# Performance work log

Hardware: AMD Instinct MI355X
Metric: run time of the kernel (lower is better)

The kernel has to match this reference:

```python
import jax, jax.numpy as jnp
import numpy as np

V, E, L, D, B, S = 50000, 512, 1024, 10, 1024, 50
N_NODES = L - 1  # internal Huffman nodes (balanced tree from uniform label counts)
LN_EPS = 1e-5
N_HIDDEN = 10


def _build_tree():
    # balanced binary tree in heap order: node at depth t for leaf l is (2^t - 1) + (l >> (D - t))
    l = np.arange(L)[:, None]
    t = np.arange(D)[None, :]
    bits = ((l >> (D - 1 - t)) & 1).astype(np.int32)          # [L, D] path direction bits
    paths = ((2 ** t - 1) + (l >> (D - t))).astype(np.int32)  # [L, D] internal node ids
    return paths, bits


def setup_inputs() -> dict:
    key = jax.random.key(0)
    k1, k2, k3, k4, k5, k6 = jax.random.split(key, 6)
    paths, bits = _build_tree()
    return {
        "input_ids": jax.random.randint(k1, (B, S), 0, V),
        "emb_table": jax.random.normal(k2, (V, E), dtype=jnp.float32) * 0.02,
        "W_h": jax.random.normal(k3, (E, E), dtype=jnp.float32) * (1.0 / np.sqrt(E)),
        "b_h": jax.random.normal(k4, (E,), dtype=jnp.float32) * 0.01,
        "theta_W": jax.random.normal(k5, (N_NODES, E, 2), dtype=jnp.float32) * (1.0 / np.sqrt(E)),
        "theta_b": jax.random.normal(k6, (N_NODES, 2), dtype=jnp.float32) * 0.01,
        "paths": jnp.asarray(paths),
        "bits": jnp.asarray(bits),
    }


def reference(input_ids, emb_table, W_h, b_h, theta_W, theta_b, paths, bits):
    # embedding + mean pool over sequence
    x = jnp.take(emb_table, input_ids, axis=0).mean(axis=1)  # [B, E]
    # LayerNorm with default (non-learned) affine, created fresh in torch forward
    mu = x.mean(axis=-1, keepdims=True)
    var = x.var(axis=-1, keepdims=True)
    x = (x - mu) * jax.lax.rsqrt(var + LN_EPS)
    # repeated hidden linear (same weights, hidden_num times)
    for _ in range(N_HIDDEN):
        x = x @ W_h + b_h
    # hierarchical softmax: batched 2-way logits at every internal node
    logits = jnp.einsum('be,ned->bnd', x, theta_W) + theta_b  # [B, N, 2]
    probs = jax.nn.softmax(logits, axis=-1)                   # [B, N, 2]
    # gather each class's path probs and multiply along the path
    p = probs[:, paths, bits]                                  # [B, L, D]
    return jnp.prod(p, axis=-1)                                # [B, L]
```

## Files before the change

kernel.cpp:

```cpp
#include <hip/hip_runtime.h>
#include <hip/hip_bf16.h>
#include <math.h>

#define B_  1024
#define S_  50
#define E_  512
#define L_  1024
#define D_  10
#define NN  1023
#define LN_EPS 1e-5f
#define CBLK 72

typedef short short8 __attribute__((ext_vector_type(8)));
typedef float f32x4  __attribute__((ext_vector_type(4)));
typedef unsigned short u16;
typedef unsigned int   u32;

union PackU { unsigned int u[4]; short8 s; };

__device__ inline void split8(const float r[8], short8& hi, short8& lo) {
    PackU H, L;
#pragma unroll
    for (int q = 0; q < 4; ++q) {
        const unsigned int u0 = __float_as_uint(r[2*q+0]);
        const unsigned int u1 = __float_as_uint(r[2*q+1]);
        H.u[q] = (u0 >> 16) | (u1 & 0xFFFF0000u);
        const float h0 = __uint_as_float(u0 & 0xFFFF0000u);
        const float h1 = __uint_as_float(u1 & 0xFFFF0000u);
        const float l0 = r[2*q+0] - h0;
        const float l1 = r[2*q+1] - h1;
        unsigned int p;
        asm("v_cvt_pk_bf16_f32 %0, %1, %2" : "=v"(p) : "v"(l0), "v"(l1));
        L.u[q] = p;
    }
    hi = H.s; lo = L.s;
}

__device__ inline void split1(float v, u16& h, u16& l) {
    const unsigned int u = __float_as_uint(v);
    h = (u16)(u >> 16);
    const float hf = __uint_as_float(u & 0xFFFF0000u);
    const float lo = v - hf;
    unsigned int p;
    asm("v_cvt_pk_bf16_f32 %0, %1, %2" : "=v"(p) : "v"(lo), "v"(lo));
    l = (u16)(p & 0xFFFFu);
}

__device__ inline void split2(float v0, float v1, u32& hw, u32& lw) {
    const unsigned int u0 = __float_as_uint(v0);
    const unsigned int u1 = __float_as_uint(v1);
    hw = (u0 >> 16) | (u1 & 0xFFFF0000u);
    const float h0 = __uint_as_float(u0 & 0xFFFF0000u);
    const float h1 = __uint_as_float(u1 & 0xFFFF0000u);
    const float l0 = v0 - h0;
    const float l1 = v1 - h1;
    asm("v_cvt_pk_bf16_f32 %0, %1, %2" : "=v"(lw) : "v"(l0), "v"(l1));
}

struct BFrag { short8 ah[2], al[2], bh[2], bl[2]; };

__device__ inline void loadB(BFrag& f,
                             const u16* pah0, const u16* pal0,
                             const u16* pah1, const u16* pal1,
                             const u16* pbh0, const u16* pbl0,
                             const u16* pbh1, const u16* pbl1, int off) {
    f.ah[0] = *reinterpret_cast<const short8*>(pah0 + off);
    f.al[0] = *reinterpret_cast<const short8*>(pal0 + off);
    f.ah[1] = *reinterpret_cast<const short8*>(pah1 + off);
    f.al[1] = *reinterpret_cast<const short8*>(pal1 + off);
    f.bh[0] = *reinterpret_cast<const short8*>(pbh0 + off);
    f.bl[0] = *reinterpret_cast<const short8*>(pbl0 + off);
    f.bh[1] = *reinterpret_cast<const short8*>(pbh1 + off);
    f.bl[1] = *reinterpret_cast<const short8*>(pbl1 + off);
}

template<int TERMS>
__device__ inline void compB(const BFrag& f, f32x4 acc[2][2]) {
#pragma unroll
    for (int i = 0; i < 2; ++i)
#pragma unroll
        for (int j = 0; j < 2; ++j) {
            acc[i][j] = __builtin_amdgcn_mfma_f32_16x16x32_bf16(f.ah[i], f.bh[j], acc[i][j], 0, 0, 0);
            acc[i][j] = __builtin_amdgcn_mfma_f32_16x16x32_bf16(f.ah[i], f.bl[j], acc[i][j], 0, 0, 0);
            acc[i][j] = __builtin_amdgcn_mfma_f32_16x16x32_bf16(f.al[i], f.bh[j], acc[i][j], 0, 0, 0);
            if (TERMS == 4)
                acc[i][j] = __builtin_amdgcn_mfma_f32_16x16x32_bf16(f.al[i], f.bl[j], acc[i][j], 0, 0, 0);
        }
}

template<int TERMS>
__device__ inline void gemmB(const u16* pah0, const u16* pal0,
                             const u16* pah1, const u16* pal1,
                             const u16* pbh0, const u16* pbl0,
                             const u16* pbh1, const u16* pbl1,
                             f32x4 acc[2][2]) {
    BFrag f0, f1;
    loadB(f0, pah0, pal0, pah1, pal1, pbh0, pbl0, pbh1, pbl1, 0);
#pragma unroll 1
    for (int kt = 0; kt < 16; kt += 2) {
        loadB(f1, pah0, pal0, pah1, pal1, pbh0, pbl0, pbh1, pbl1, (kt + 1) * 32);
        compB<TERMS>(f0, acc);
        if (kt + 2 < 16) loadB(f0, pah0, pal0, pah1, pal1, pbh0, pbl0, pbh1, pbl1, (kt + 2) * 32);
        compB<TERMS>(f1, acc);
    }
}

__device__ inline void do_embed_row(const int* __restrict__ ids,
                                    const float* __restrict__ emb,
                                    u16* __restrict__ xah, u16* __restrict__ xal, int b) {
    const int t = threadIdx.x;
    float a0 = 0.f, a1 = 0.f;
    const int* idr = ids + b * S_;
#pragma unroll 5
    for (int s = 0; s < S_; ++s) {
        const float2 v = *reinterpret_cast<const float2*>(emb + (long)idr[s] * E_ + 2 * t);
        a0 += v.x;
        a1 += v.y;
    }
    a0 *= (1.f / S_);
    a1 *= (1.f / S_);

    __shared__ float red[256];
    red[t] = a0 + a1;
    __syncthreads();
    for (int off = 128; off > 0; off >>= 1) {
        if (t < off) red[t] += red[t + off];
        __syncthreads();
    }
    const float mean = red[0] * (1.f / E_);
    __syncthreads();
    const float d0 = a0 - mean, d1 = a1 - mean;
    red[t] = d0 * d0 + d1 * d1;
    __syncthreads();
    for (int off = 128; off > 0; off >>= 1) {
        if (t < off) red[t] += red[t + off];
        __syncthreads();
    }
    const float var = red[0] * (1.f / E_);
    const float inv = 1.f / sqrtf(var + LN_EPS);
    u32 hw, lw;
    split2(d0 * inv, d1 * inv, hw, lw);
    *reinterpret_cast<u32*>(xah + (long)b * E_ + 2 * t) = hw;
    *reinterpret_cast<u32*>(xal + (long)b * E_ + 2 * t) = lw;
}

__device__ inline void do_dpack(const float* __restrict__ thW,
                                u16* __restrict__ Dh, u16* __restrict__ Dl, int part) {
    const int total = NN * 256;
    const int nth = 64 * 256;
    for (int p = part * 256 + (int)threadIdx.x; p < total; p += nth) {
        const int n = p >> 8;
        const int kp = p & 255;
        const float4 v = *reinterpret_cast<const float4*>(thW + (long)n * 1024 + kp * 4);
        u32 hw, lw;
        split2(v.y - v.x, v.w - v.z, hw, lw);
        *reinterpret_cast<u32*>(Dh + (long)n * E_ + kp * 2) = hw;
        *reinterpret_cast<u32*>(Dl + (long)n * E_ + kp * 2) = lw;
    }
}

__device__ inline void compose_epilogue(f32x4 acc[2][2], int row_base, int col_base,
                                        int kg, int r_lo,
                                        const float* __restrict__ Bbias,
                                        u16* __restrict__ Ch, u16* __restrict__ Cl,
                                        u16* __restrict__ Th, u16* __restrict__ Tl,
                                        float* __restrict__ cvec) {
#pragma unroll
    for (int j = 0; j < 2; ++j) {
        const int col = col_base + j * 16 + r_lo;
        const float bb = Bbias[col];
#pragma unroll
        for (int i = 0; i < 2; ++i) {
            const int row0 = row_base + i * 16 + kg * 4;
            union { ushort4 v; u16 e[4]; } th, tl;
#pragma unroll
            for (int r2 = 0; r2 < 4; ++r2) {
                const int row = row0 + r2;
                float v = acc[i][j][r2];
                if (row == E_) { v += bb; cvec[col] = v; }
                u16 h, l;
                split1(v, h, l);
                if (row <= E_ && Ch != nullptr) {
                    Ch[(long)row * E_ + col] = h;
                    Cl[(long)row * E_ + col] = l;
                }
                th.e[r2] = h; tl.e[r2] = l;
            }
            if (row0 + 3 < E_) {
                *reinterpret_cast<ushort4*>(Th + (long)col * E_ + row0) = th.v;
                *reinterpret_cast<ushort4*>(Tl + (long)col * E_ + row0) = tl.v;
            }
        }
    }
}

__device__ inline void do_compose0(const float* __restrict__ Wh, const float* __restrict__ bh,
                                   u16* __restrict__ Ch, u16* __restrict__ Cl,
                                   u16* __restrict__ Th, u16* __restrict__ Tl,
                                   float* __restrict__ cvec, int bid) {
    const int tid  = threadIdx.x;
    const int wid  = tid >> 6;
    const int lane = tid & 63;
    const int r_lo = lane & 15;
    const int kg   = lane >> 4;
    const int row_base = (bid >> 3) * 64 + (wid >> 1) * 32;
    const int col_base = (bid & 7) * 64 + (wid & 1) * 32;
    f32x4 acc[2][2] = {};
#pragma unroll 2
    for (int kt = 0; kt < E_; kt += 32) {
        const int ks = kt + kg * 8;
        short8 ah[2], al[2], bhf[2], blf[2];
#pragma unroll
        for (int i = 0; i < 2; ++i) {
            const int row = row_base + i * 16 + r_lo;
            const float* ap = (row < E_) ? (Wh + (long)row * E_ + ks) : (bh + ks);
            const float4 v0 = *reinterpret_cast<const float4*>(ap);
            const float4 v1 = *reinterpret_cast<const float4*>(ap + 4);
            const float rr[8] = {v0.x, v0.y, v0.z, v0.w, v1.x, v1.y, v1.z, v1.w};
            split8(rr, ah[i], al[i]);
        }
#pragma unroll
        for (int j = 0; j < 2; ++j) {
            const int c = col_base + j * 16 + r_lo;
            float rr[8];
#pragma unroll
            for (int q = 0; q < 8; ++q) rr[q] = Wh[(long)(ks + q) * E_ + c];
            split8(rr, bhf[j], blf[j]);
        }
#pragma unroll
        for (int i = 0; i < 2; ++i)
#pragma unroll
            for (int j = 0; j < 2; ++j) {
                acc[i][j] = __builtin_amdgcn_mfma_f32_16x16x32_bf16(ah[i], bhf[j], acc[i][j], 0, 0, 0);
                acc[i][j] = __builtin_amdgcn_mfma_f32_16x16x32_bf16(ah[i], blf[j], acc[i][j], 0, 0, 0);
                acc[i][j] = __builtin_amdgcn_mfma_f32_16x16x32_bf16(al[i], bhf[j], acc[i][j], 0, 0, 0);
                acc[i][j] = __builtin_amdgcn_mfma_f32_16x16x32_bf16(al[i], blf[j], acc[i][j], 0, 0, 0);
            }
    }
    compose_epilogue(acc, row_base, col_base, kg, r_lo, bh, Ch, Cl, Th, Tl, cvec);
}

__device__ inline void do_composeB(const u16* __restrict__ Ah, const u16* __restrict__ Al,
                                   const u16* __restrict__ Bh, const u16* __restrict__ Bl,
                                   const float* __restrict__ Bbias,
                                   u16* __restrict__ Ch, u16* __restrict__ Cl,
                                   u16* __restrict__ Th, u16* __restrict__ Tl,
                                   float* __restrict__ cvec, int bid) {
    const int tid  = threadIdx.x;
    const int wid  = tid >> 6;
    const int lane = tid & 63;
    const int r_lo = lane & 15;
    const int kg   = lane >> 4;
    const int row_base = (bid >> 3) * 64 + (wid >> 1) * 32;
    const int col_base = (bid & 7) * 64 + (wid & 1) * 32;

    int ra0 = row_base + r_lo;        if (ra0 > E_) ra0 = E_;
    int ra1 = row_base + 16 + r_lo;   if (ra1 > E_) ra1 = E_;
    const long rb0 = col_base + r_lo;
    const long rb1 = col_base + 16 + r_lo;

    f32x4 acc[2][2] = {};
    gemmB<4>(Ah + (long)ra0 * E_ + kg * 8, Al + (long)ra0 * E_ + kg * 8,
             Ah + (long)ra1 * E_ + kg * 8, Al + (long)ra1 * E_ + kg * 8,
             Bh + rb0 * E_ + kg * 8,       Bl + rb0 * E_ + kg * 8,
             Bh + rb1 * E_ + kg * 8,       Bl + rb1 * E_ + kg * 8, acc);

    compose_epilogue(acc, row_base, col_base, kg, r_lo, Bbias, Ch, Cl, Th, Tl, cvec);
}

__device__ inline void do_applyB(const u16* __restrict__ Xh, const u16* __restrict__ Xl,
                                 const u16* __restrict__ Mh, const u16* __restrict__ Ml,
                                 const float* __restrict__ cvec,
                                 u16* __restrict__ Yh, u16* __restrict__ Yl,
                                 int tr, int tc) {
    const int tid  = threadIdx.x;
    const int wid  = tid >> 6;
    const int lane = tid & 63;
    const int r_lo = lane & 15;
    const int kg   = lane >> 4;
    const int row_base = tr * 64 + (wid >> 1) * 32;
    const int col_base = tc * 64 + (wid & 1) * 32;

    const long ra0 = row_base + r_lo;
    const long ra1 = row_base + 16 + r_lo;
    const long rb0 = col_base + r_lo;
    const long rb1 = col_base + 16 + r_lo;

    f32x4 acc[2][2] = {};
    gemmB<3>(Xh + ra0 * E_ + kg * 8, Xl + ra0 * E_ + kg * 8,
             Xh + ra1 * E_ + kg * 8, Xl + ra1 * E_ + kg * 8,
             Mh + rb0 * E_ + kg * 8, Ml + rb0 * E_ + kg * 8,
             Mh + rb1 * E_ + kg * 8, Ml + rb1 * E_ + kg * 8, acc);

#pragma unroll
    for (int j = 0; j < 2; ++j) {
        const int col = col_base + j * 16 + r_lo;
        const float bb = cvec[col];
#pragma unroll
        for (int i = 0; i < 2; ++i) {
#pragma unroll
            for (int r2 = 0; r2 < 4; ++r2) {
                const int row = row_base + i * 16 + kg * 4 + r2;
                u16 h, l;
                split1(acc[i][j][r2] + bb, h, l);
                Yh[(long)row * E_ + col] = h;
                Yl[(long)row * E_ + col] = l;
            }
        }
    }
}

__global__ __launch_bounds__(256) void k_fused0(const float* __restrict__ Wh,
                                                const float* __restrict__ bh,
                                                u16* __restrict__ Ch0, u16* __restrict__ Cl0,
                                                u16* __restrict__ Th0, u16* __restrict__ Tl0,
                                                float* __restrict__ cvec0,
                                                const int* __restrict__ ids,
                                                const float* __restrict__ emb,
                                                u16* __restrict__ xah, u16* __restrict__ xal,
                                                const float* __restrict__ thW,
                                                u16* __restrict__ Dh, u16* __restrict__ Dl) {
    const int bid = blockIdx.x;
    if (bid < CBLK)             do_compose0(Wh, bh, Ch0, Cl0, Th0, Tl0, cvec0, bid);
    else if (bid < CBLK + 1024) do_embed_row(ids, emb, xah, xal, bid - CBLK);
    else                        do_dpack(thW, Dh, Dl, bid - CBLK - 1024);
}

__global__ __launch_bounds__(256) void k_fused1(const u16* __restrict__ Ch0, const u16* __restrict__ Cl0,
                                                const u16* __restrict__ Th0, const u16* __restrict__ Tl0,
                                                const float* __restrict__ cvec0,
                                                u16* __restrict__ Th1, u16* __restrict__ Tl1,
                                                float* __restrict__ cvec1,
                                                const u16* __restrict__ xah, const u16* __restrict__ xal,
                                                u16* __restrict__ y1h, u16* __restrict__ y1l) {
    const int bid = blockIdx.x;
    if (bid < CBLK) {
        do_composeB(Ch0, Cl0, Th0, Tl0, cvec0, nullptr, nullptr, Th1, Tl1, cvec1, bid);
    } else {
        const int t = bid - CBLK;
        do_applyB(xah, xal, Th0, Tl0, cvec0, y1h, y1l, t >> 3, t & 7);
    }
}

__global__ __launch_bounds__(256) void k_apply(const u16* __restrict__ Yh, const u16* __restrict__ Yl,
                                               const u16* __restrict__ Th1, const u16* __restrict__ Tl1,
                                               const float* __restrict__ cvec1,
                                               u16* __restrict__ Zh, u16* __restrict__ Zl) {
    do_applyB(Yh, Yl, Th1, Tl1, cvec1, Zh, Zl, blockIdx.x >> 3, blockIdx.x & 7);
}

__global__ __launch_bounds__(256) void k_theta_sig(const u16* __restrict__ Xh, const u16* __restrict__ Xl,
                                                   const u16* __restrict__ Dh, const u16* __restrict__ Dl,
                                                   const float* __restrict__ thb,
                                                   float* __restrict__ sig) {
    const int tid  = threadIdx.x;
    const int wid  = tid >> 6;
    const int lane = tid & 63;
    const int r_lo = lane & 15;
    const int kg   = lane >> 4;
    const int tr = blockIdx.x >> 4;
    const int tc = blockIdx.x & 15;
    const int row_base = tr * 64 + (wid >> 1) * 32;
    const int col_base = tc * 64 + (wid & 1) * 32;

    long c0 = col_base + r_lo;        if (c0 > NN - 1) c0 = NN - 1;
    long c1 = col_base + 16 + r_lo;   if (c1 > NN - 1) c1 = NN - 1;
    const long ra0 = row_base + r_lo;
    const long ra1 = row_base + 16 + r_lo;

    f32x4 acc[2][2] = {};
    gemmB<3>(Xh + ra0 * E_ + kg * 8, Xl + ra0 * E_ + kg * 8,
             Xh + ra1 * E_ + kg * 8, Xl + ra1 * E_ + kg * 8,
             Dh + c0 * E_ + kg * 8,  Dl + c0 * E_ + kg * 8,
             Dh + c1 * E_ + kg * 8,  Dl + c1 * E_ + kg * 8, acc);

#pragma unroll
    for (int j = 0; j < 2; ++j) {
        const int col = col_base + j * 16 + r_lo;
        const int cc = (col > NN - 1) ? (NN - 1) : col;
        const float g = thb[2 * cc + 1] - thb[2 * cc + 0];
#pragma unroll
        for (int i = 0; i < 2; ++i) {
#pragma unroll
            for (int r2 = 0; r2 < 4; ++r2) {
                const int row = row_base + i * 16 + kg * 4 + r2;
                if (col < NN) {
                    const float z = acc[i][j][r2] + g;
                    sig[(long)row * 1024 + col] = 1.f / (1.f + __expf(-z));
                }
            }
        }
    }
}

__global__ __launch_bounds__(256) void k_leaf_gather(const float* __restrict__ sig,
                                                     float* __restrict__ out) {
    __shared__ float s[1024];
    const int b = blockIdx.x;
    const int tid = threadIdx.x;
    reinterpret_cast<float4*>(s)[tid] =
        reinterpret_cast<const float4*>(sig + (long)b * 1024)[tid];
    __syncthreads();
    float* orow = out + (long)b * L_;
#pragma unroll 1
    for (int q = 0; q < 4; ++q) {
        const int l = q * 256 + tid;
        float p = 1.f;
#pragma unroll
        for (int t = 0; t < D_; ++t) {
            const int node = (1 << t) - 1 + (l >> (D_ - t));
            const int bit  = (l >> (D_ - 1 - t)) & 1;
            const float sv = s[node];
            p *= bit ? sv : (1.f - sv);
        }
        orow[l] = p;
    }
}

extern "C" void kernel_launch(void* const* d_in, const int* in_sizes, int n_in,
                              void* d_out, int out_size, void* d_ws, size_t ws_size,
                              hipStream_t stream) {
    const int*   ids = (const int*)d_in[0];
    const float* emb = (const float*)d_in[1];
    const float* Wh  = (const float*)d_in[2];
    const float* bh  = (const float*)d_in[3];
    const float* thW = (const float*)d_in[4];
    const float* thb = (const float*)d_in[5];
    float* out = (float*)d_out;

    char* ws = (char*)d_ws;
    const size_t MB = 1u << 20;
    u16* xah = (u16*)(ws + 0 * MB);
    u16* xal = (u16*)(ws + 1 * MB);
    u16* y1h = (u16*)(ws + 2 * MB);
    u16* y1l = (u16*)(ws + 3 * MB);
    u16* y2h = (u16*)(ws + 4 * MB);
    u16* y2l = (u16*)(ws + 5 * MB);
    u16* y3h = (u16*)(ws + 6 * MB);
    u16* y3l = (u16*)(ws + 7 * MB);
    float* sig = (float*)(ws + 8 * MB);
    u16* Dh  = (u16*)(ws + 12 * MB);
    u16* Dl  = (u16*)(ws + 13 * MB);
    u16* Ch0 = (u16*)(ws + 14 * MB);
    u16* Cl0 = (u16*)(ws + 15 * MB);
    u16* Th0 = (u16*)(ws + 16 * MB);
    u16* Tl0 = (u16*)(ws + 16 * MB + 512 * 1024);
    u16* Th1 = (u16*)(ws + 17 * MB);
    u16* Tl1 = (u16*)(ws + 17 * MB + 512 * 1024);
    float* cvec0 = (float*)(ws + 18 * MB);
    float* cvec1 = (float*)(ws + 18 * MB + 4096);

    k_fused0<<<CBLK + 1024 + 64, 256, 0, stream>>>(Wh, bh, Ch0, Cl0, Th0, Tl0, cvec0,
                                                   ids, emb, xah, xal, thW, Dh, Dl);

    k_fused1<<<CBLK + 128, 256, 0, stream>>>(Ch0, Cl0, Th0, Tl0, cvec0,
                                             Th1, Tl1, cvec1,
                                             xah, xal, y1h, y1l);

    k_apply<<<128, 256, 0, stream>>>(y1h, y1l, Th1, Tl1, cvec1, y2h, y2l);

    k_apply<<<128, 256, 0, stream>>>(y2h, y2l, Th1, Tl1, cvec1, y3h, y3l);

    k_theta_sig<<<256, 256, 0, stream>>>(y3h, y3l, Dh, Dl, thb, sig);

    k_leaf_gather<<<B_, 256, 0, stream>>>(sig, out);
}
```

Baseline: 100.5 us.

## Split-K the apply and theta GEMMs into two halves with fp32 partial outputs

The apply and theta GEMMs now split K=512 into two halves, doubling the block count (128→256, 256→512) so more CUs are busy. Each half writes an fp32 partial, and the next stage sums the two partials and splits to bf16 hi/lo inside the GEMM load path. The theta bias is precomputed into gvec and the sigmoid moves into the leaf-gather kernel, which sums the partials. This trades higher occupancy for twice the fp32 intermediate traffic and extra conversion work in each GEMM.

Result: slower. 108.5 us (+7.9%).

```diff
diff --git a/kernel.cpp b/kernel.cpp
--- a/kernel.cpp
+++ b/kernel.cpp
@@ -88,7 +88,7 @@
         }
 }
 
-template<int TERMS>
+template<int TERMS, int CHUNKS>
 __device__ inline void gemmB(const u16* pah0, const u16* pal0,
                              const u16* pah1, const u16* pal1,
                              const u16* pbh0, const u16* pbl0,
@@ -97,11 +97,68 @@
     BFrag f0, f1;
     loadB(f0, pah0, pal0, pah1, pal1, pbh0, pbl0, pbh1, pbl1, 0);
 #pragma unroll 1
-    for (int kt = 0; kt < 16; kt += 2) {
+    for (int kt = 0; kt < CHUNKS; kt += 2) {
         loadB(f1, pah0, pal0, pah1, pal1, pbh0, pbl0, pbh1, pbl1, (kt + 1) * 32);
         compB<TERMS>(f0, acc);
-        if (kt + 2 < 16) loadB(f0, pah0, pal0, pah1, pal1, pbh0, pbl0, pbh1, pbl1, (kt + 2) * 32);
+        if (kt + 2 < CHUNKS) loadB(f0, pah0, pal0, pah1, pal1, pbh0, pbl0, pbh1, pbl1, (kt + 2) * 32);
         compB<TERMS>(f1, acc);
+    }
+}
+
+struct FPFrag { float aA[2][8], aB[2][8]; short8 bh[2], bl[2]; };
+
+__device__ inline void loadFP(FPFrag& f,
+                              const float* pa0A, const float* pa0B,
+                              const float* pa1A, const float* pa1B,
+                              const u16* pbh0, const u16* pbl0,
+                              const u16* pbh1, const u16* pbl1, int off) {
+    *reinterpret_cast<float4*>(&f.aA[0][0]) = *reinterpret_cast<const float4*>(pa0A + off);
+    *reinterpret_cast<float4*>(&f.aA[0][4]) = *reinterpret_cast<const float4*>(pa0A + off + 4);
+    *reinterpret_cast<float4*>(&f.aB[0][0]) = *reinterpret_cast<const float4*>(pa0B + off);
+    *reinterpret_cast<float4*>(&f.aB[0][4]) = *reinterpret_cast<const float4*>(pa0B + off + 4);
+    *reinterpret_cast<float4*>(&f.aA[1][0]) = *reinterpret_cast<const float4*>(pa1A + off);
+    *reinterpret_cast<float4*>(&f.aA[1][4]) = *reinterpret_cast<const float4*>(pa1A + off + 4);
+    *reinterpret_cast<float4*>(&f.aB[1][0]) = *reinterpret_cast<const float4*>(pa1B + off);
+    *reinterpret_cast<float4*>(&f.aB[1][4]) = *reinterpret_cast<const float4*>(pa1B + off + 4);
+    f.bh[0] = *reinterpret_cast<const short8*>(pbh0 + off);
+    f.bl[0] = *reinterpret_cast<const short8*>(pbl0 + off);
+    f.bh[1] = *reinterpret_cast<const short8*>(pbh1 + off);
+    f.bl[1] = *reinterpret_cast<const short8*>(pbl1 + off);
+}
+
+__device__ inline void compFP(const FPFrag& f, f32x4 acc[2][2]) {
+    short8 ah[2], al[2];
+#pragma unroll
+    for (int i = 0; i < 2; ++i) {
+        float rr[8];
+#pragma unroll
+        for (int q = 0; q < 8; ++q) rr[q] = f.aA[i][q] + f.aB[i][q];
+        split8(rr, ah[i], al[i]);
+    }
+#pragma unroll
+    for (int i = 0; i < 2; ++i)
+#pragma unroll
+        for (int j = 0; j < 2; ++j) {
+            acc[i][j] = __builtin_amdgcn_mfma_f32_16x16x32_bf16(ah[i], f.bh[j], acc[i][j], 0, 0, 0);
+            acc[i][j] = __builtin_amdgcn_mfma_f32_16x16x32_bf16(ah[i], f.bl[j], acc[i][j], 0, 0, 0);
+            acc[i][j] = __builtin_amdgcn_mfma_f32_16x16x32_bf16(al[i], f.bh[j], acc[i][j], 0, 0, 0);
+        }
+}
+
+template<int CHUNKS>
+__device__ inline void gemmFP(const float* pa0A, const float* pa0B,
+                              const float* pa1A, const float* pa1B,
+                              const u16* pbh0, const u16* pbl0,
+                              const u16* pbh1, const u16* pbl1,
+                              f32x4 acc[2][2]) {
+    FPFrag f0, f1;
+    loadFP(f0, pa0A, pa0B, pa1A, pa1B, pbh0, pbl0, pbh1, pbl1, 0);
+#pragma unroll 1
+    for (int kt = 0; kt < CHUNKS; kt += 2) {
+        loadFP(f1, pa0A, pa0B, pa1A, pa1B, pbh0, pbl0, pbh1, pbl1, (kt + 1) * 32);
+        compFP(f0, acc);
+        if (kt + 2 < CHUNKS) loadFP(f0, pa0A, pa0B, pa1A, pa1B, pbh0, pbl0, pbh1, pbl1, (kt + 2) * 32);
+        compFP(f1, acc);
     }
 }
 
@@ -145,10 +202,16 @@
 }
 
 __device__ inline void do_dpack(const float* __restrict__ thW,
-                                u16* __restrict__ Dh, u16* __restrict__ Dl, int part) {
+                                u16* __restrict__ Dh, u16* __restrict__ Dl,
+                                const float* __restrict__ thb,
+                                float* __restrict__ gvec, int part) {
+    const int tid = threadIdx.x;
+    const int p0 = part * 256 + tid;
+    if (p0 < NN)       gvec[p0] = thb[2 * p0 + 1] - thb[2 * p0];
+    else if (p0 == NN) gvec[p0] = 0.f;
     const int total = NN * 256;
     const int nth = 64 * 256;
-    for (int p = part * 256 + (int)threadIdx.x; p < total; p += nth) {
+    for (int p = p0; p < total; p += nth) {
         const int n = p >> 8;
         const int kp = p & 255;
         const float4 v = *reinterpret_cast<const float4*>(thW + (long)n * 1024 + kp * 4);
@@ -260,54 +323,12 @@
     const long rb1 = col_base + 16 + r_lo;
 
     f32x4 acc[2][2] = {};
-    gemmB<4>(Ah + (long)ra0 * E_ + kg * 8, Al + (long)ra0 * E_ + kg * 8,
-             Ah + (long)ra1 * E_ + kg * 8, Al + (long)ra1 * E_ + kg * 8,
-             Bh + rb0 * E_ + kg * 8,       Bl + rb0 * E_ + kg * 8,
-             Bh + rb1 * E_ + kg * 8,       Bl + rb1 * E_ + kg * 8, acc);
+    gemmB<4, 16>(Ah + (long)ra0 * E_ + kg * 8, Al + (long)ra0 * E_ + kg * 8,
+                 Ah + (long)ra1 * E_ + kg * 8, Al + (long)ra1 * E_ + kg * 8,
+                 Bh + rb0 * E_ + kg * 8,       Bl + rb0 * E_ + kg * 8,
+                 Bh + rb1 * E_ + kg * 8,       Bl + rb1 * E_ + kg * 8, acc);
 
     compose_epilogue(acc, row_base, col_base, kg, r_lo, Bbias, Ch, Cl, Th, Tl, cvec);
-}
-
-__device__ inline void do_applyB(const u16* __restrict__ Xh, const u16* __restrict__ Xl,
-                                 const u16* __restrict__ Mh, const u16* __restrict__ Ml,
-                                 const float* __restrict__ cvec,
-                                 u16* __restrict__ Yh, u16* __restrict__ Yl,
-                                 int tr, int tc) {
-    const int tid  = threadIdx.x;
-    const int wid  = tid >> 6;
-    const int lane = tid & 63;
-    const int r_lo = lane & 15;
-    const int kg   = lane >> 4;
-    const int row_base = tr * 64 + (wid >> 1) * 32;
-    const int col_base = tc * 64 + (wid & 1) * 32;
-
-    const long ra0 = row_base + r_lo;
-    const long ra1 = row_base + 16 + r_lo;
-    const long rb0 = col_base + r_lo;
-    const long rb1 = col_base + 16 + r_lo;
-
-    f32x4 acc[2][2] = {};
-    gemmB<3>(Xh + ra0 * E_ + kg * 8, Xl + ra0 * E_ + kg * 8,
-             Xh + ra1 * E_ + kg * 8, Xl + ra1 * E_ + kg * 8,
-             Mh + rb0 * E_ + kg * 8, Ml + rb0 * E_ + kg * 8,
-             Mh + rb1 * E_ + kg * 8, Ml + rb1 * E_ + kg * 8, acc);
-
-#pragma unroll
-    for (int j = 0; j < 2; ++j) {
-        const int col = col_base + j * 16 + r_lo;
-        const float bb = cvec[col];
-#pragma unroll
-        for (int i = 0; i < 2; ++i) {
-#pragma unroll
-            for (int r2 = 0; r2 < 4; ++r2) {
-                const int row = row_base + i * 16 + kg * 4 + r2;
-                u16 h, l;
-                split1(acc[i][j][r2] + bb, h, l);
-                Yh[(long)row * E_ + col] = h;
-                Yl[(long)row * E_ + col] = l;
-            }
-        }
-    }
 }
 
 __global__ __launch_bounds__(256) void k_fused0(const float* __restrict__ Wh,
@@ -319,11 +340,13 @@
                                                 const float* __restrict__ emb,
                                                 u16* __restrict__ xah, u16* __restrict__ xal,
                                                 const float* __restrict__ thW,
-                                                u16* __restrict__ Dh, u16* __restrict__ Dl) {
+                                                u16* __restrict__ Dh, u16* __restrict__ Dl,
+                                                const float* __restrict__ thb,
+                                                float* __restrict__ gvec) {
     const int bid = blockIdx.x;
     if (bid < CBLK)             do_compose0(Wh, bh, Ch0, Cl0, Th0, Tl0, cvec0, bid);
     else if (bid < CBLK + 1024) do_embed_row(ids, emb, xah, xal, bid - CBLK);
-    else                        do_dpack(thW, Dh, Dl, bid - CBLK - 1024);
+    else                        do_dpack(thW, Dh, Dl, thb, gvec, bid - CBLK - 1024);
 }
 
 __global__ __launch_bounds__(256) void k_fused1(const u16* __restrict__ Ch0, const u16* __restrict__ Cl0,
@@ -332,36 +355,104 @@
                                                 u16* __restrict__ Th1, u16* __restrict__ Tl1,
                                                 float* __restrict__ cvec1,
                                                 const u16* __restrict__ xah, const u16* __restrict__ xal,
-                                                u16* __restrict__ y1h, u16* __restrict__ y1l) {
+                                                float* __restrict__ y1A, float* __restrict__ y1B) {
     const int bid = blockIdx.x;
     if (bid < CBLK) {
         do_composeB(Ch0, Cl0, Th0, Tl0, cvec0, nullptr, nullptr, Th1, Tl1, cvec1, bid);
-    } else {
-        const int t = bid - CBLK;
-        do_applyB(xah, xal, Th0, Tl0, cvec0, y1h, y1l, t >> 3, t & 7);
-    }
-}
-
-__global__ __launch_bounds__(256) void k_apply(const u16* __restrict__ Yh, const u16* __restrict__ Yl,
-                                               const u16* __restrict__ Th1, const u16* __restrict__ Tl1,
-                                               const float* __restrict__ cvec1,
-                                               u16* __restrict__ Zh, u16* __restrict__ Zl) {
-    do_applyB(Yh, Yl, Th1, Tl1, cvec1, Zh, Zl, blockIdx.x >> 3, blockIdx.x & 7);
-}
-
-__global__ __launch_bounds__(256) void k_theta_sig(const u16* __restrict__ Xh, const u16* __restrict__ Xl,
-                                                   const u16* __restrict__ Dh, const u16* __restrict__ Dl,
-                                                   const float* __restrict__ thb,
-                                                   float* __restrict__ sig) {
+        return;
+    }
+    const int t    = bid - CBLK;
+    const int kk   = t >> 7;
+    const int tile = t & 127;
+    const int koff = kk * 256;
     const int tid  = threadIdx.x;
     const int wid  = tid >> 6;
     const int lane = tid & 63;
     const int r_lo = lane & 15;
     const int kg   = lane >> 4;
-    const int tr = blockIdx.x >> 4;
-    const int tc = blockIdx.x & 15;
-    const int row_base = tr * 64 + (wid >> 1) * 32;
-    const int col_base = tc * 64 + (wid & 1) * 32;
+    const int row_base = (tile >> 3) * 64 + (wid >> 1) * 32;
+    const int col_base = (tile & 7) * 64 + (wid & 1) * 32;
+    const long ra0 = row_base + r_lo;
+    const long ra1 = row_base + 16 + r_lo;
+    const long rb0 = col_base + r_lo;
+    const long rb1 = col_base + 16 + r_lo;
+
+    f32x4 acc[2][2] = {};
+    gemmB<3, 8>(xah + ra0 * E_ + koff + kg * 8, xal + ra0 * E_ + koff + kg * 8,
+                xah + ra1 * E_ + koff + kg * 8, xal + ra1 * E_ + koff + kg * 8,
+                Th0 + rb0 * E_ + koff + kg * 8, Tl0 + rb0 * E_ + koff + kg * 8,
+                Th0 + rb1 * E_ + koff + kg * 8, Tl0 + rb1 * E_ + koff + kg * 8, acc);
+
+    float* Y = kk ? y1B : y1A;
+#pragma unroll
+    for (int j = 0; j < 2; ++j) {
+        const int col = col_base + j * 16 + r_lo;
+        const float bb = kk ? cvec0[col] : 0.f;
+#pragma unroll
+        for (int i = 0; i < 2; ++i)
+#pragma unroll
+            for (int r2 = 0; r2 < 4; ++r2) {
+                const int row = row_base + i * 16 + kg * 4 + r2;
+                Y[(long)row * E_ + col] = acc[i][j][r2] + bb;
+            }
+    }
+}
+
+__global__ __launch_bounds__(256) void k_applyFP(const float* __restrict__ XA, const float* __restrict__ XB,
+                                                 const u16* __restrict__ Mh, const u16* __restrict__ Ml,
+                                                 const float* __restrict__ cvec,
+                                                 float* __restrict__ YA, float* __restrict__ YB) {
+    const int bid  = blockIdx.x;
+    const int kk   = bid >> 7;
+    const int tile = bid & 127;
+    const int koff = kk * 256;
+    const int tid  = threadIdx.x;
+    const int wid  = tid >> 6;
+    const int lane = tid & 63;
+    const int r_lo = lane & 15;
+    const int kg   = lane >> 4;
+    const int row_base = (tile >> 3) * 64 + (wid >> 1) * 32;
+    const int col_base = (tile & 7) * 64 + (wid & 1) * 32;
+    const long ra0 = row_base + r_lo;
+    const long ra1 = row_base + 16 + r_lo;
+    const long rb0 = col_base + r_lo;
+    const long rb1 = col_base + 16 + r_lo;
+
+    f32x4 acc[2][2] = {};
+    gemmFP<8>(XA + ra0 * E_ + koff + kg * 8, XB + ra0 * E_ + koff + kg * 8,
+              XA + ra1 * E_ + koff + kg * 8, XB + ra1 * E_ + koff + kg * 8,
+              Mh + rb0 * E_ + koff + kg * 8, Ml + rb0 * E_ + koff + kg * 8,
+              Mh + rb1 * E_ + koff + kg * 8, Ml + rb1 * E_ + koff + kg * 8, acc);
+
+    float* Y = kk ? YB : YA;
+#pragma unroll
+    for (int j = 0; j < 2; ++j) {
+        const int col = col_base + j * 16 + r_lo;
+        const float bb = kk ? cvec[col] : 0.f;
+#pragma unroll
+        for (int i = 0; i < 2; ++i)
+#pragma unroll
+            for (int r2 = 0; r2 < 4; ++r2) {
+                const int row = row_base + i * 16 + kg * 4 + r2;
+                Y[(long)row * E_ + col] = acc[i][j][r2] + bb;
+            }
+    }
+}
+
+__global__ __launch_bounds__(256) void k_thetaFP(const float* __restrict__ XA, const float* __restrict__ XB,
+                                                 const u16* __restrict__ Dh, const u16* __restrict__ Dl,
+                                                 float* __restrict__ sgA, float* __restrict__ sgB) {
+    const int bid  = blockIdx.x;
+    const int kk   = bid >> 8;
+    const int tile = bid & 255;
+    const int koff = kk * 256;
+    const int tid  = threadIdx.x;
+    const int wid  = tid >> 6;
+    const int lane = tid & 63;
+    const int r_lo = lane & 15;
+    const int kg   = lane >> 4;
+    const int row_base = (tile >> 4) * 64 + (wid >> 1) * 32;
+    const int col_base = (tile & 15) * 64 + (wid & 1) * 32;
 
     long c0 = col_base + r_lo;        if (c0 > NN - 1) c0 = NN - 1;
     long c1 = col_base + 16 + r_lo;   if (c1 > NN - 1) c1 = NN - 1;
@@ -369,37 +460,43 @@
     const long ra1 = row_base + 16 + r_lo;
 
     f32x4 acc[2][2] = {};
-    gemmB<3>(Xh + ra0 * E_ + kg * 8, Xl + ra0 * E_ + kg * 8,
-             Xh + ra1 * E_ + kg * 8, Xl + ra1 * E_ + kg * 8,
-             Dh + c0 * E_ + kg * 8,  Dl + c0 * E_ + kg * 8,
-             Dh + c1 * E_ + kg * 8,  Dl + c1 * E_ + kg * 8, acc);
-
+    gemmFP<8>(XA + ra0 * E_ + koff + kg * 8, XB + ra0 * E_ + koff + kg * 8,
+              XA + ra1 * E_ + koff + kg * 8, XB + ra1 * E_ + koff + kg * 8,
+              Dh + c0 * E_ + koff + kg * 8,  Dl + c0 * E_ + koff + kg * 8,
+              Dh + c1 * E_ + koff + kg * 8,  Dl + c1 * E_ + koff + kg * 8, acc);
+
+    float* S = kk ? sgB : sgA;
 #pragma unroll
     for (int j = 0; j < 2; ++j) {
         const int col = col_base + j * 16 + r_lo;
-        const int cc = (col > NN - 1) ? (NN - 1) : col;
-        const float g = thb[2 * cc + 1] - thb[2 * cc + 0];
-#pragma unroll
-        for (int i = 0; i < 2; ++i) {
+#pragma unroll
+        for (int i = 0; i < 2; ++i)
 #pragma unroll
             for (int r2 = 0; r2 < 4; ++r2) {
                 const int row = row_base + i * 16 + kg * 4 + r2;
                 if (col < NN) {
-                    const float z = acc[i][j][r2] + g;
-                    sig[(long)row * 1024 + col] = 1.f / (1.f + __expf(-z));
+                    S[(long)row * 1024 + col] = acc[i][j][r2];
                 }
             }
-        }
-    }
-}
-
-__global__ __launch_bounds__(256) void k_leaf_gather(const float* __restrict__ sig,
-                                                     float* __restrict__ out) {
+    }
+}
+
+__global__ __launch_bounds__(256) void k_leaf2(const float* __restrict__ sgA,
+                                               const float* __restrict__ sgB,
+                                               const float* __restrict__ gvec,
+                                               float* __restrict__ out) {
     __shared__ float s[1024];
     const int b = blockIdx.x;
     const int tid = threadIdx.x;
-    reinterpret_cast<float4*>(s)[tid] =
-        reinterpret_cast<const float4*>(sig + (long)b * 1024)[tid];
+    const float4 a = reinterpret_cast<const float4*>(sgA + (long)b * 1024)[tid];
+    const float4 c = reinterpret_cast<const float4*>(sgB + (long)b * 1024)[tid];
+    const float4 g = reinterpret_cast<const float4*>(gvec)[tid];
+    float4 r;
+    r.x = 1.f / (1.f + __expf(-(a.x + c.x + g.x)));
+    r.y = 1.f / (1.f + __expf(-(a.y + c.y + g.y)));
+    r.z = 1.f / (1.f + __expf(-(a.z + c.z + g.z)));
+    r.w = 1.f / (1.f + __expf(-(a.w + c.w + g.w)));
+    reinterpret_cast<float4*>(s)[tid] = r;
     __syncthreads();
     float* orow = out + (long)b * L_;
 #pragma unroll 1
@@ -432,36 +529,39 @@
     const size_t MB = 1u << 20;
     u16* xah = (u16*)(ws + 0 * MB);
     u16* xal = (u16*)(ws + 1 * MB);
-    u16* y1h = (u16*)(ws + 2 * MB);
-    u16* y1l = (u16*)(ws + 3 * MB);
-    u16* y2h = (u16*)(ws + 4 * MB);
-    u16* y2l = (u16*)(ws + 5 * MB);
-    u16* y3h = (u16*)(ws + 6 * MB);
-    u16* y3l = (u16*)(ws + 7 * MB);
-    float* sig = (float*)(ws + 8 * MB);
-    u16* Dh  = (u16*)(ws + 12 * MB);
-    u16* Dl  = (u16*)(ws + 13 * MB);
-    u16* Ch0 = (u16*)(ws + 14 * MB);
-    u16* Cl0 = (u16*)(ws + 15 * MB);
-    u16* Th0 = (u16*)(ws + 16 * MB);
-    u16* Tl0 = (u16*)(ws + 16 * MB + 512 * 1024);
-    u16* Th1 = (u16*)(ws + 17 * MB);
-    u16* Tl1 = (u16*)(ws + 17 * MB + 512 * 1024);
-    float* cvec0 = (float*)(ws + 18 * MB);
-    float* cvec1 = (float*)(ws + 18 * MB + 4096);
+    float* y1A = (float*)(ws + 2 * MB);
+    float* y1B = (float*)(ws + 4 * MB);
+    float* y2A = (float*)(ws + 6 * MB);
+    float* y2B = (float*)(ws + 8 * MB);
+    float* y3A = (float*)(ws + 10 * MB);
+    float* y3B = (float*)(ws + 12 * MB);
+    float* sgA = (float*)(ws + 14 * MB);
+    float* sgB = (float*)(ws + 18 * MB);
+    u16* Dh  = (u16*)(ws + 22 * MB);
+    u16* Dl  = (u16*)(ws + 23 * MB);
+    u16* Ch0 = (u16*)(ws + 24 * MB);
+    u16* Cl0 = (u16*)(ws + 25 * MB);
+    u16* Th0 = (u16*)(ws + 26 * MB);
+    u16* Tl0 = (u16*)(ws + 26 * MB + 512 * 1024);
+    u16* Th1 = (u16*)(ws + 27 * MB);
+    u16* Tl1 = (u16*)(ws + 27 * MB + 512 * 1024);
+    float* cvec0 = (float*)(ws + 28 * MB);
+    float* cvec1 = (float*)(ws + 28 * MB + 4096);
+    float* gvec  = (float*)(ws + 28 * MB + 8192);
 
     k_fused0<<<CBLK + 1024 + 64, 256, 0, stream>>>(Wh, bh, Ch0, Cl0, Th0, Tl0, cvec0,
-                                                   ids, emb, xah, xal, thW, Dh, Dl);
-
-    k_fused1<<<CBLK + 128, 256, 0, stream>>>(Ch0, Cl0, Th0, Tl0, cvec0,
+                                                   ids, emb, xah, xal, thW, Dh, Dl,
+                                                   thb, gvec);
+
+    k_fused1<<<CBLK + 256, 256, 0, stream>>>(Ch0, Cl0, Th0, Tl0, cvec0,
                                              Th1, Tl1, cvec1,
-                                             xah, xal, y1h, y1l);
-
-    k_apply<<<128, 256, 0, stream>>>(y1h, y1l, Th1, Tl1, cvec1, y2h, y2l);
-
-    k_apply<<<128, 256, 0, stream>>>(y2h, y2l, Th1, Tl1, cvec1, y3h, y3l);
-
-    k_theta_sig<<<256, 256, 0, stream>>>(y3h, y3l, Dh, Dl, thb, sig);
-
-    k_leaf_gather<<<B_, 256, 0, stream>>>(sig, out);
-}
+                                             xah, xal, y1A, y1B);
+
+    k_applyFP<<<256, 256, 0, stream>>>(y1A, y1B, Th1, Tl1, cvec1, y2A, y2B);
+
+    k_applyFP<<<256, 256, 0, stream>>>(y2A, y2B, Th1, Tl1, cvec1, y3A, y3B);
+
+    k_thetaFP<<<512, 256, 0, stream>>>(y3A, y3B, Dh, Dl, sgA, sgB);
+
+    k_leaf2<<<B_, 256, 0, stream>>>(sgA, sgB, gvec, out);
+}
```

## Fold final hidden-layer power into theta difference matrix to drop one apply launch

Applied to the files above, without the earlier changes.

Composes the augmented power of the hidden affine map with the theta difference matrix, running concurrently with the second apply in a new fused kernel, so the last apply kernel is eliminated. The theta bias difference is precomputed during dpack and folded into a per-node bias vector. This removes one dependent launch and one B×E×E GEMM pass, adding a 512×1023 compose GEMM that overlaps with the apply. It also changes the rounding path, since the hi/lo split is applied to the composed matrix.

Measured after the change: 98.05 us, median of 2. 2.5% less time.

```diff
diff --git a/kernel.cpp b/kernel.cpp
--- a/kernel.cpp
+++ b/kernel.cpp
@@ -10,6 +10,7 @@
 #define NN  1023
 #define LN_EPS 1e-5f
 #define CBLK 72
+#define DBLK 144
 
 typedef short short8 __attribute__((ext_vector_type(8)));
 typedef float f32x4  __attribute__((ext_vector_type(4)));
@@ -145,10 +146,16 @@
 }
 
 __device__ inline void do_dpack(const float* __restrict__ thW,
-                                u16* __restrict__ Dh, u16* __restrict__ Dl, int part) {
+                                u16* __restrict__ Dh, u16* __restrict__ Dl,
+                                const float* __restrict__ thb,
+                                float* __restrict__ gvec, int part) {
+    const int tid = threadIdx.x;
+    const int p0 = part * 256 + tid;
+    if (p0 < NN)       gvec[p0] = thb[2 * p0 + 1] - thb[2 * p0];
+    else if (p0 == NN) gvec[p0] = 0.f;
     const int total = NN * 256;
     const int nth = 64 * 256;
-    for (int p = part * 256 + (int)threadIdx.x; p < total; p += nth) {
+    for (int p = p0; p < total; p += nth) {
         const int n = p >> 8;
         const int kp = p & 255;
         const float4 v = *reinterpret_cast<const float4*>(thW + (long)n * 1024 + kp * 4);
@@ -268,6 +275,55 @@
     compose_epilogue(acc, row_base, col_base, kg, r_lo, Bbias, Ch, Cl, Th, Tl, cvec);
 }
 
+__device__ inline void do_composeD(const u16* __restrict__ Ah, const u16* __restrict__ Al,
+                                   const u16* __restrict__ Dh, const u16* __restrict__ Dl,
+                                   const float* __restrict__ gvec,
+                                   u16* __restrict__ Lh, u16* __restrict__ Ll,
+                                   float* __restrict__ gg, int bid) {
+    const int tid  = threadIdx.x;
+    const int wid  = tid >> 6;
+    const int lane = tid & 63;
+    const int r_lo = lane & 15;
+    const int kg   = lane >> 4;
+    const int row_base = (bid >> 4) * 64 + (wid >> 1) * 32;
+    const int col_base = (bid & 15) * 64 + (wid & 1) * 32;
+
+    int ra0 = row_base + r_lo;        if (ra0 > E_) ra0 = E_;
+    int ra1 = row_base + 16 + r_lo;   if (ra1 > E_) ra1 = E_;
+    long c0 = col_base + r_lo;        if (c0 > NN - 1) c0 = NN - 1;
+    long c1 = col_base + 16 + r_lo;   if (c1 > NN - 1) c1 = NN - 1;
+
+    f32x4 acc[2][2] = {};
+    gemmB<4>(Ah + (long)ra0 * E_ + kg * 8, Al + (long)ra0 * E_ + kg * 8,
+             Ah + (long)ra1 * E_ + kg * 8, Al + (long)ra1 * E_ + kg * 8,
+             Dh + c0 * E_ + kg * 8,        Dl + c0 * E_ + kg * 8,
+             Dh + c1 * E_ + kg * 8,        Dl + c1 * E_ + kg * 8, acc);
+
+#pragma unroll
+    for (int j = 0; j < 2; ++j) {
+        const int col = col_base + j * 16 + r_lo;
+        const float bb = (col < NN) ? gvec[col] : 0.f;
+#pragma unroll
+        for (int i = 0; i < 2; ++i) {
+            const int row0 = row_base + i * 16 + kg * 4;
+            union { ushort4 v; u16 e[4]; } th, tl;
+#pragma unroll
+            for (int r2 = 0; r2 < 4; ++r2) {
+                const int row = row0 + r2;
+                float v = acc[i][j][r2];
+                if (row == E_) { v += bb; if (col < NN) gg[col] = v; }
+                u16 h, l;
+                split1(v, h, l);
+                th.e[r2] = h; tl.e[r2] = l;
+            }
+            if (row0 + 3 < E_ && col < NN) {
+                *reinterpret_cast<ushort4*>(Lh + (long)col * E_ + row0) = th.v;
+                *reinterpret_cast<ushort4*>(Ll + (long)col * E_ + row0) = tl.v;
+            }
+        }
+    }
+}
+
 __device__ inline void do_applyB(const u16* __restrict__ Xh, const u16* __restrict__ Xl,
                                  const u16* __restrict__ Mh, const u16* __restrict__ Ml,
                                  const float* __restrict__ cvec,
@@ -319,39 +375,53 @@
                                                 const float* __restrict__ emb,
                                                 u16* __restrict__ xah, u16* __restrict__ xal,
                                                 const float* __restrict__ thW,
-                                                u16* __restrict__ Dh, u16* __restrict__ Dl) {
+                                                u16* __restrict__ Dh, u16* __restrict__ Dl,
+                                                const float* __restrict__ thb,
+                                                float* __restrict__ gvec) {
     const int bid = blockIdx.x;
     if (bid < CBLK)             do_compose0(Wh, bh, Ch0, Cl0, Th0, Tl0, cvec0, bid);
     else if (bid < CBLK + 1024) do_embed_row(ids, emb, xah, xal, bid - CBLK);
-    else                        do_dpack(thW, Dh, Dl, bid - CBLK - 1024);
+    else                        do_dpack(thW, Dh, Dl, thb, gvec, bid - CBLK - 1024);
 }
 
 __global__ __launch_bounds__(256) void k_fused1(const u16* __restrict__ Ch0, const u16* __restrict__ Cl0,
                                                 const u16* __restrict__ Th0, const u16* __restrict__ Tl0,
                                                 const float* __restrict__ cvec0,
+                                                u16* __restrict__ Ch1, u16* __restrict__ Cl1,
                                                 u16* __restrict__ Th1, u16* __restrict__ Tl1,
                                                 float* __restrict__ cvec1,
                                                 const u16* __restrict__ xah, const u16* __restrict__ xal,
                                                 u16* __restrict__ y1h, u16* __restrict__ y1l) {
     const int bid = blockIdx.x;
     if (bid < CBLK) {
-        do_composeB(Ch0, Cl0, Th0, Tl0, cvec0, nullptr, nullptr, Th1, Tl1, cvec1, bid);
+        do_composeB(Ch0, Cl0, Th0, Tl0, cvec0, Ch1, Cl1, Th1, Tl1, cvec1, bid);
     } else {
         const int t = bid - CBLK;
         do_applyB(xah, xal, Th0, Tl0, cvec0, y1h, y1l, t >> 3, t & 7);
     }
 }
 
-__global__ __launch_bounds__(256) void k_apply(const u16* __restrict__ Yh, const u16* __restrict__ Yl,
-                                               const u16* __restrict__ Th1, const u16* __restrict__ Tl1,
-                                               const float* __restrict__ cvec1,
-                                               u16* __restrict__ Zh, u16* __restrict__ Zl) {
-    do_applyB(Yh, Yl, Th1, Tl1, cvec1, Zh, Zl, blockIdx.x >> 3, blockIdx.x & 7);
+__global__ __launch_bounds__(256) void k_fused2(const u16* __restrict__ Ch1, const u16* __restrict__ Cl1,
+                                                const u16* __restrict__ Th1, const u16* __restrict__ Tl1,
+                                                const float* __restrict__ cvec1,
+                                                const u16* __restrict__ Dh, const u16* __restrict__ Dl,
+                                                const float* __restrict__ gvec,
+                                                u16* __restrict__ Lh, u16* __restrict__ Ll,
+                                                float* __restrict__ gg,
+                                                const u16* __restrict__ y1h, const u16* __restrict__ y1l,
+                                                u16* __restrict__ y2h, u16* __restrict__ y2l) {
+    const int bid = blockIdx.x;
+    if (bid < DBLK) {
+        do_composeD(Ch1, Cl1, Dh, Dl, gvec, Lh, Ll, gg, bid);
+    } else {
+        const int t = bid - DBLK;
+        do_applyB(y1h, y1l, Th1, Tl1, cvec1, y2h, y2l, t >> 3, t & 7);
+    }
 }
 
 __global__ __launch_bounds__(256) void k_theta_sig(const u16* __restrict__ Xh, const u16* __restrict__ Xl,
-                                                   const u16* __restrict__ Dh, const u16* __restrict__ Dl,
-                                                   const float* __restrict__ thb,
+                                                   const u16* __restrict__ Lh, const u16* __restrict__ Ll,
+                                                   const float* __restrict__ gg,
                                                    float* __restrict__ sig) {
     const int tid  = threadIdx.x;
     const int wid  = tid >> 6;
@@ -371,21 +441,21 @@
     f32x4 acc[2][2] = {};
     gemmB<3>(Xh + ra0 * E_ + kg * 8, Xl + ra0 * E_ + kg * 8,
              Xh + ra1 * E_ + kg * 8, Xl + ra1 * E_ + kg * 8,
-             Dh + c0 * E_ + kg * 8,  Dl + c0 * E_ + kg * 8,
-             Dh + c1 * E_ + kg * 8,  Dl + c1 * E_ + kg * 8, acc);
+             Lh + c0 * E_ + kg * 8,  Ll + c0 * E_ + kg * 8,
+             Lh + c1 * E_ + kg * 8,  Ll + c1 * E_ + kg * 8, acc);
 
 #pragma unroll
     for (int j = 0; j < 2; ++j) {
         const int col = col_base + j * 16 + r_lo;
         const int cc = (col > NN - 1) ? (NN - 1) : col;
-        const float g = thb[2 * cc + 1] - thb[2 * cc + 0];
+        const float bb = gg[cc];
 #pragma unroll
         for (int i = 0; i < 2; ++i) {
 #pragma unroll
             for (int r2 = 0; r2 < 4; ++r2) {
                 const int row = row_base + i * 16 + kg * 4 + r2;
                 if (col < NN) {
-                    const float z = acc[i][j][r2] + g;
+                    const float z = acc[i][j][r2] + bb;
                     sig[(long)row * 1024 + col] = 1.f / (1.f + __expf(-z));
                 }
             }
@@ -436,32 +506,37 @@
     u16* y1l = (u16*)(ws + 3 * MB);
     u16* y2h = (u16*)(ws + 4 * MB);
     u16* y2l = (u16*)(ws + 5 * MB);
-    u16* y3h = (u16*)(ws + 6 * MB);
-    u16* y3l = (u16*)(ws + 7 * MB);
-    float* sig = (float*)(ws + 8 * MB);
-    u16* Dh  = (u16*)(ws + 12 * MB);
-    u16* Dl  = (u16*)(ws + 13 * MB);
-    u16* Ch0 = (u16*)(ws + 14 * MB);
-    u16* Cl0 = (u16*)(ws + 15 * MB);
+    float* sig = (float*)(ws + 6 * MB);
+    u16* Dh  = (u16*)(ws + 10 * MB);
+    u16* Dl  = (u16*)(ws + 11 * MB);
+    u16* Ch0 = (u16*)(ws + 12 * MB);
+    u16* Cl0 = (u16*)(ws + 13 * MB);
+    u16* Ch1 = (u16*)(ws + 14 * MB);
+    u16* Cl1 = (u16*)(ws + 15 * MB);
     u16* Th0 = (u16*)(ws + 16 * MB);
     u16* Tl0 = (u16*)(ws + 16 * MB + 512 * 1024);
     u16* Th1 = (u16*)(ws + 17 * MB);
     u16* Tl1 = (u16*)(ws + 17 * MB + 512 * 1024);
-    float* cvec0 = (float*)(ws + 18 * MB);
-    float* cvec1 = (float*)(ws + 18 * MB + 4096);
+    u16* Lh  = (u16*)(ws + 18 * MB);
+    u16* Ll  = (u16*)(ws + 19 * MB);
+    float* cvec0 = (float*)(ws + 20 * MB);
+    float* cvec1 = (float*)(ws + 20 * MB + 4096);
+    float* gvec  = (float*)(ws + 20 * MB + 8192);
+    float* gg    = (float*)(ws + 20 * MB + 12288);
 
     k_fused0<<<CBLK + 1024 + 64, 256, 0, stream>>>(Wh, bh, Ch0, Cl0, Th0, Tl0, cvec0,
-                                                   ids, emb, xah, xal, thW, Dh, Dl);
+                                                   ids, emb, xah, xal, thW, Dh, Dl,
+                                                   thb, gvec);
 
     k_fused1<<<CBLK + 128, 256, 0, stream>>>(Ch0, Cl0, Th0, Tl0, cvec0,
-                                             Th1, Tl1, cvec1,
+                                             Ch1, Cl1, Th1, Tl1, cvec1,
                                              xah, xal, y1h, y1l);
 
-    k_apply<<<128, 256, 0, stream>>>(y1h, y1l, Th1, Tl1, cvec1, y2h, y2l);
-
-    k_apply<<<128, 256, 0, stream>>>(y2h, y2l, Th1, Tl1, cvec1, y3h, y3l);
-
-    k_theta_sig<<<256, 256, 0, stream>>>(y3h, y3l, Dh, Dl, thb, sig);
+    k_fused2<<<DBLK + 128, 256, 0, stream>>>(Ch1, Cl1, Th1, Tl1, cvec1,
+                                             Dh, Dl, gvec, Lh, Ll, gg,
+                                             y1h, y1l, y2h, y2l);
+
+    k_theta_sig<<<256, 256, 0, stream>>>(y2h, y2l, Lh, Ll, gg, sig);
 
     k_leaf_gather<<<B_, 256, 0, stream>>>(sig, out);
 }
```
